# Performance work log

Measured on AMD Instinct MI355X. Metric: run time of the kernel, lower is better.

Reference implementation:

```python
import jax, jax.numpy as jnp
import numpy as np

TW = 25          # time_window
H = 128          # hidden_features
NL = 6           # hidden_layer
N = 8192         # batch*n_nodes
E = 131072       # edges (avg degree 16)
EDGE_DIM = 51    # 50 (u diff) + 1 (pos_x diff)
LEM_IN = 4       # pos_x, u_ch0, u_ch1, ts
PDE_L = 16.0
PDE_TMAX = 4.0
PDE_DT = 0.04
NEG_SLOPE = 0.2  # PyG GATConv leaky_relu slope


def swish(x):
    return x * jax.nn.sigmoid(x)


def setup_inputs() -> dict:
    key = jax.random.key(0)
    ks = jax.random.split(key, 32)
    def p(k, shape, s=0.05):
        return jax.random.normal(k, shape, jnp.float32) * s
    inp = {}
    inp['u'] = jax.random.normal(ks[0], (N, 2 * TW), jnp.float32)
    inp['pos'] = jax.random.uniform(ks[1], (N, 2), jnp.float32)
    inp['edge_index'] = jax.random.randint(ks[2], (2, E), 0, N)
    # LEM cell params (inp2hid: 4H, hid2hid: 3H, transform_z: H)
    inp['lem_inp_w'] = p(ks[3], (4 * H, LEM_IN)); inp['lem_inp_b'] = jnp.zeros(4 * H, jnp.float32)
    inp['lem_hid_w'] = p(ks[4], (3 * H, H));      inp['lem_hid_b'] = jnp.zeros(3 * H, jnp.float32)
    inp['lem_z_w'] = p(ks[5], (H, H));            inp['lem_z_b'] = jnp.zeros(H, jnp.float32)
    # lemoutput_mlp
    inp['mlp1_w'] = p(ks[6], (H, H)); inp['mlp1_b'] = jnp.zeros(H, jnp.float32)
    inp['mlp2_w'] = p(ks[7], (H, H)); inp['mlp2_b'] = jnp.zeros(H, jnp.float32)
    # main GAT layers (stacked over NL)
    inp['gnn_lin_w'] = p(ks[8], (NL, H, H)); inp['gnn_edge_w'] = p(ks[9], (NL, H, EDGE_DIM))
    inp['gnn_att_src'] = p(ks[10], (NL, H)); inp['gnn_att_dst'] = p(ks[11], (NL, H))
    inp['gnn_att_edge'] = p(ks[12], (NL, H)); inp['gnn_bias'] = jnp.zeros((NL, H), jnp.float32)
    # gate GAT layers
    inp['gate_lin_w'] = p(ks[13], (NL, H, H)); inp['gate_edge_w'] = p(ks[14], (NL, H, EDGE_DIM))
    inp['gate_att_src'] = p(ks[15], (NL, H)); inp['gate_att_dst'] = p(ks[16], (NL, H))
    inp['gate_att_edge'] = p(ks[17], (NL, H)); inp['gate_bias'] = jnp.zeros((NL, H), jnp.float32)
    # double_mlp + conv1d decoder (time_window==25 branch)
    inp['dbl_w'] = p(ks[18], (2 * H, H)); inp['dbl_b'] = jnp.zeros(2 * H, jnp.float32)
    inp['conv1_w'] = p(ks[19], (8, 2, 16)); inp['conv1_b'] = jnp.zeros(8, jnp.float32)
    inp['conv2_w'] = p(ks[20], (2, 8, 14)); inp['conv2_b'] = jnp.zeros(2, jnp.float32)
    return inp


def _gat(x, src, dst, edge_attr, lin_w, edge_w, a_src, a_dst, a_edge, bias):
    """Single-head GATConv with edge features (PyG semantics, aggregate at dst)."""
    xt = x @ lin_w.T                      # [N,H]
    et = edge_attr @ edge_w.T             # [E,H]
    logits = jax.nn.leaky_relu((xt @ a_src)[src] + (xt @ a_dst)[dst] + et @ a_edge, NEG_SLOPE)
    amax = jax.ops.segment_max(logits, dst, num_segments=N)
    amax = jnp.where(jnp.isfinite(amax), amax, 0.0)
    ex = jnp.exp(logits - amax[dst])
    denom = jax.ops.segment_sum(ex, dst, num_segments=N)
    w = ex / (denom[dst] + 1e-16)         # edge softmax over incoming edges
    out = jax.ops.segment_sum(w[:, None] * xt[src], dst, num_segments=N)
    return out + bias


def _forward(u, pos, lem_inp_w, lem_inp_b, lem_hid_w, lem_hid_b, lem_z_w, lem_z_b,
             mlp1_w, mlp1_b, mlp2_w, mlp2_b,
             gnn_lin_w, gnn_edge_w, gnn_att_src, gnn_att_dst, gnn_att_edge, gnn_bias,
             gate_lin_w, gate_edge_w, gate_att_src, gate_att_dst, gate_att_edge, gate_bias,
             dbl_w, dbl_b, conv1_w, conv1_b, conv2_w, conv2_b, edge_index):
    pos_x = pos[:, 1:2] / PDE_L    # [N,1]
    pos_t = pos[:, 0:1] / PDE_TMAX # [N,1]
    dt = jnp.cumsum(jnp.full((TW,), PDE_DT, jnp.float32))  # [TW]
    ts = pos_t + dt[None, :]       # [N,TW]
    # LEM input: [TW, N, 4] = (pos_x, u channel 0, u channel 1, ts)
    lem_x = jnp.concatenate([
        jnp.broadcast_to(pos_x[None, :, :], (TW, N, 1)),
        u[:, :TW].T[:, :, None],
        u[:, TW:].T[:, :, None],
        ts.T[:, :, None],
    ], axis=-1)

    def cell(carry, xt):
        y, z = carry
        ii = xt @ lem_inp_w.T + lem_inp_b   # [N,4H]
        hh = y @ lem_hid_w.T + lem_hid_b    # [N,3H]
        i1, i2, i3, i4 = jnp.split(ii, 4, axis=-1)
        h1, h2, h3 = jnp.split(hh, 3, axis=-1)
        ms_dt_bar = jax.nn.sigmoid(i1 + h1)
        ms_dt = jax.nn.sigmoid(i2 + h2)
        z = (1.0 - ms_dt) * z + ms_dt * jnp.tanh(i3 + h3)
        y = (1.0 - ms_dt_bar) * y + ms_dt_bar * jnp.tanh(z @ lem_z_w.T + lem_z_b + i4)
        return (y, z), None

    y0 = jnp.zeros((N, H), u.dtype)
    (y, _), _ = jax.lax.scan(cell, (y0, y0), lem_x)
    h = swish(y @ mlp1_w.T + mlp1_b)
    h = swish(h @ mlp2_w.T + mlp2_b)

    src, dst = edge_index[0], edge_index[1]
    edge_attr = jnp.concatenate([u[src] - u[dst], pos_x[src] - pos_x[dst]], axis=-1)  # [E,51]

    for i in range(NL):
        tau = jax.nn.sigmoid(_gat(h, src, dst, edge_attr, gate_lin_w[i], gate_edge_w[i],
                                  gate_att_src[i], gate_att_dst[i], gate_att_edge[i], gate_bias[i]))
        msg = swish(_gat(h, src, dst, edge_attr, gnn_lin_w[i], gnn_edge_w[i],
                         gnn_att_src[i], gnn_att_dst[i], gnn_att_edge[i], gnn_bias[i]))
        h = (1.0 - tau) * h + tau * msg

    h2 = swish(h @ dbl_w.T + dbl_b).reshape(N, 2, H)  # [N,2,128]
    dn = ('NCH', 'OIH', 'NCH')
    d = jax.lax.conv_general_dilated(h2, conv1_w, (3,), 'VALID', dimension_numbers=dn)
    d = swish(d + conv1_b[None, :, None])              # [N,8,38]
    d = jax.lax.conv_general_dilated(d, conv2_w, (1,), 'VALID', dimension_numbers=dn)
    d = d + conv2_b[None, :, None]                     # [N,2,25]
    out = u.reshape(N, 2, TW) + dt[None, None, :] * d
    return out.reshape(N, 2 * TW)


def reference(u, pos, edge_index, lem_inp_w, lem_inp_b, lem_hid_w, lem_hid_b, lem_z_w, lem_z_b,
              mlp1_w, mlp1_b, mlp2_w, mlp2_b,
              gnn_lin_w, gnn_edge_w, gnn_att_src, gnn_att_dst, gnn_att_edge, gnn_bias,
              gate_lin_w, gate_edge_w, gate_att_src, gate_att_dst, gate_att_edge, gate_bias,
              dbl_w, dbl_b, conv1_w, conv1_b, conv2_w, conv2_b):
    return _forward(u, pos, lem_inp_w, lem_inp_b, lem_hid_w, lem_hid_b, lem_z_w, lem_z_b,
                    mlp1_w, mlp1_b, mlp2_w, mlp2_b,
                    gnn_lin_w, gnn_edge_w, gnn_att_src, gnn_att_dst, gnn_att_edge, gnn_bias,
                    gate_lin_w, gate_edge_w, gate_att_src, gate_att_dst, gate_att_edge, gate_bias,
                    dbl_w, dbl_b, conv1_w, conv1_b, conv2_w, conv2_b, edge_index)
```

## Files before the change

kernel.cpp:

```cpp
#include <hip/hip_runtime.h>

#define N_NODES 8192
#define N_EDGES 131072

using short8 = __attribute__((ext_vector_type(8))) short;
using f32x4  = __attribute__((ext_vector_type(4))) float;

__device__ __forceinline__ float rcpf(float x){ return __builtin_amdgcn_rcpf(x); }
__device__ __forceinline__ float sigm(float x){ return rcpf(1.0f+__expf(-x)); }
__device__ __forceinline__ float ftanh(float x){ float e=__expf(2.0f*x); return (e-1.0f)*rcpf(e+1.0f); }
__device__ __forceinline__ float swishf(float x){ return x*sigm(x); }
__device__ __forceinline__ float leaky(float x){ return x>=0.0f? x : 0.2f*x; }
__device__ __forceinline__ float dot4(float4 a, float4 b){ return a.x*b.x+a.y*b.y+a.z*b.z+a.w*b.w; }
__device__ __forceinline__ short f2bf(float x){
  unsigned u=__float_as_uint(x);
  unsigned r=(u + 0x7fffu + ((u>>16)&1u))>>16;
  return (short)r;
}
__device__ __forceinline__ int cvtpk(float a, float b){
  int r; asm("v_cvt_pk_bf16_f32 %0, %1, %2" : "=v"(r) : "v"(a), "v"(b)); return r;
}

__device__ __forceinline__ float wave_rsum(float v){
  #pragma unroll
  for(int m=32;m;m>>=1) v+=__shfl_xor(v,m);
  return v;
}

__global__ __launch_bounds__(256) void hist_kernel(const int* __restrict__ dst, int* __restrict__ cnt){
  int e=blockIdx.x*256+threadIdx.x;
  if(e<N_EDGES) atomicAdd(&cnt[dst[e]],1);
}

__global__ __launch_bounds__(1024) void scan_kernel(const int* __restrict__ cnt, int* __restrict__ rowptr, int* __restrict__ cursor){
  __shared__ int sums[1024];
  int t=threadIdx.x; int base=t*8;
  int local[8]; int s=0;
  #pragma unroll
  for(int i=0;i<8;++i){ local[i]=s; s+=cnt[base+i]; }
  sums[t]=s; __syncthreads();
  for(int off=1;off<1024;off<<=1){
    int v=(t>=off)?sums[t-off]:0;
    __syncthreads();
    sums[t]+=v;
    __syncthreads();
  }
  int offset=(t>0)?sums[t-1]:0;
  #pragma unroll
  for(int i=0;i<8;++i){ int v=offset+local[i]; rowptr[base+i]=v; cursor[base+i]=v; }
  if(t==1023) rowptr[N_NODES]=sums[1023];
}

__global__ __launch_bounds__(256) void scatter_kernel(const int* __restrict__ src, const int* __restrict__ dst,
                                                      int* __restrict__ cursor, int* __restrict__ csr_src){
  int e=blockIdx.x*256+threadIdx.x;
  if(e<N_EDGES){
    int slot=atomicAdd(&cursor[dst[e]],1);
    csr_src[slot]=src[e];
  }
}

__global__ __launch_bounds__(256) void prep_bf16_kernel(
    const float* __restrict__ lem_hid_w, const float* __restrict__ lem_z_w,
    const float* __restrict__ mlp1_w, const float* __restrict__ mlp2_w,
    const float* __restrict__ gate_lin_w, const float* __restrict__ gnn_lin_w,
    const float* __restrict__ gate_ew, const float* __restrict__ gnn_ew,
    const float* __restrict__ gate_ae, const float* __restrict__ gnn_ae,
    short* __restrict__ whb, short* __restrict__ wzb, short* __restrict__ w1b,
    short* __restrict__ w2b, short* __restrict__ wlin16, float* __restrict__ we)
{
  int i=blockIdx.x*256+threadIdx.x;
  if(i<49152){ whb[i]=f2bf(lem_hid_w[i]); return; }
  if(i<65536){ int k=i-49152; wzb[k]=f2bf(lem_z_w[k]); return; }
  if(i<81920){ int k=i-65536; w1b[k]=f2bf(mlp1_w[k]); return; }
  if(i<98304){ int k=i-81920; w2b[k]=f2bf(mlp2_w[k]); return; }
  if(i<294912){
    int k=i-98304;
    int l=k>>15, which=(k>>14)&1, r=k&16383;
    const float* s = which? gnn_lin_w + l*16384 + r : gate_lin_w + l*16384 + r;
    wlin16[k]=f2bf(*s);
    return;
  }
  int idx=i-294912;
  if(idx>=12*51) return;
  int g=idx/51, k=idx%51, l=g>>1;
  const float* ew = (g&1)? gnn_ew + l*128*51 : gate_ew + l*128*51;
  const float* ae = (g&1)? gnn_ae + l*128    : gate_ae + l*128;
  float s=0.f;
  for(int f=0;f<128;++f) s+=ew[f*51+k]*ae[f];
  we[idx]=s;
}

__global__ __launch_bounds__(128) void gsc_kernel(const float* __restrict__ u, const float* __restrict__ pos,
                                                  const float* __restrict__ we, float* __restrict__ gsc){
  int n=blockIdx.x*128+threadIdx.x;
  float uv[50];
  #pragma unroll
  for(int k=0;k<50;++k) uv[k]=u[n*50+k];
  float px=pos[n*2+1]*(1.0f/16.0f);
  for(int g=0;g<12;++g){
    const float* w=we+g*51;
    float s=w[50]*px;
    #pragma unroll
    for(int k=0;k<50;++k) s+=w[k]*uv[k];
    gsc[g*N_NODES+n]=s;
  }
}

__device__ __forceinline__ void transform_phase(
    int tid, int n0,
    const short* __restrict__ h16, short* __restrict__ xts,
    float* __restrict__ ssred, float* __restrict__ sdred,
    const short* __restrict__ wl,
    const float* __restrict__ a_sg, const float* __restrict__ a_dg,
    const float* __restrict__ a_sm, const float* __restrict__ a_dm,
    const float* __restrict__ gsc_g, const float* __restrict__ gsc_m,
    short* __restrict__ xt_out, float* __restrict__ ss_out, float* __restrict__ sd_out)
{
  const int lane=tid&63, w=tid>>6;
  const int cg=w&1, ch=w>>1;
  const int r16=lane&15, kq=lane>>4;
  __syncthreads();
  short8 afr[4];
  #pragma unroll
  for(int kk=0;kk<4;++kk)
    afr[kk]=*(const short8*)&h16[r16*128 + ((kk*32+kq*8) ^ ((r16&7)<<3))];
  const short* wb = wl + cg*16384;
  const float* as_ = cg? a_sm : a_sg;
  const float* ad_ = cg? a_dm : a_dg;
  float ssp[4]={0,0,0,0}, sdp[4]={0,0,0,0};
  #pragma unroll
  for(int ci=0;ci<2;++ci){
    int c0=(ch*2+ci)*16;
    f32x4 acc={0.f,0.f,0.f,0.f};
    #pragma unroll
    for(int kk=0;kk<4;++kk){
      short8 b=*(const short8*)(wb + (c0+r16)*128 + kk*32 + kq*8);
      acc=__builtin_amdgcn_mfma_f32_16x16x32_bf16(afr[kk],b,acc,0,0,0);
    }
    float av=as_[c0+r16], dv=ad_[c0+r16];
    #pragma unroll
    for(int r=0;r<4;++r){
      ssp[r]+=acc[r]*av; sdp[r]+=acc[r]*dv;
      xts[(kq*4+r)*256 + cg*128 + c0 + r16]=f2bf(acc[r]);
    }
  }
  #pragma unroll
  for(int m=1;m<16;m<<=1){
    #pragma unroll
    for(int r=0;r<4;++r){ ssp[r]+=__shfl_xor(ssp[r],m); sdp[r]+=__shfl_xor(sdp[r],m); }
  }
  if(r16==0){
    #pragma unroll
    for(int r=0;r<4;++r){ ssred[w*16+kq*4+r]=ssp[r]; sdred[w*16+kq*4+r]=sdp[r]; }
  }
  __syncthreads();
  if(tid<32){
    int node=tid&15, cg2=tid>>4;
    float sv=0.f, dv=0.f;
    #pragma unroll
    for(int c2=0;c2<4;++c2){ sv+=ssred[(c2*2+cg2)*16+node]; dv+=sdred[(c2*2+cg2)*16+node]; }
    float gv=(cg2? gsc_m:gsc_g)[n0+node];
    ss_out[2*(n0+node)+cg2]=sv+gv;
    sd_out[2*(n0+node)+cg2]=dv-gv;
  }
  {
    const short8* sp=(const short8*)xts;
    short8* dp=(short8*)(xt_out + (size_t)n0*256);
    dp[tid]=sp[tid];
  }
}

__device__ __forceinline__ float4 aggregate_node(
    int n, int lane, float4* __restrict__ stgw,
    const int* __restrict__ rowptr, const int* __restrict__ csr_src,
    const short* __restrict__ xt_in, const float* __restrict__ ss_in, const float* __restrict__ sd_in,
    const float* __restrict__ bias_g, const float* __restrict__ bias_m,
    const float* __restrict__ h)
{
  const int s0=rowptr[n], deg=rowptr[n+1]-s0;
  const float2 sdv=*(const float2*)(sd_in+2*n);
  const float bg=sdv.x, bm=sdv.y;
  float4 hv={0.f,0.f,0.f,0.f};
  if(lane<32) hv=*(const float4*)(h + (size_t)n*128 + 4*lane);
  float dg=0.f,dm=0.f, acc0=0.f,acc1=0.f,acc2=0.f,acc3=0.f;
  for(int c=0;c<deg;c+=64){
    int i=c+lane, s=0; float eg=0.f, em=0.f;
    if(i<deg){
      s=csr_src[s0+i];
      float2 ssv=*(const float2*)(ss_in+2*s);
      eg=__expf(fminf(leaky(ssv.x+bg),60.f));
      em=__expf(fminf(leaky(ssv.y+bm),60.f));
      dg+=eg; dm+=em;
    }
    float4 st; st.x=__int_as_float(s); st.y=eg; st.z=em; st.w=0.f;
    stgw[lane]=st;
    __threadfence_block();
    int cnt=min(64,deg-c);
    for(int cb=0;cb<cnt;cb+=16){
      int sj[16]; float wj[16];
      #pragma unroll
      for(int j=0;j<16;++j){
        int idx=cb+j;
        float4 ev=stgw[idx<cnt? idx : cb];
        sj[j]=__float_as_int(ev.x);
        wj[j]=(idx<cnt)? (lane<32? ev.y : ev.z) : 0.f;
      }
      uint2 rows[16];
      #pragma unroll
      for(int j=0;j<16;++j)
        rows[j]=*(const uint2*)(xt_in + (size_t)sj[j]*256 + 4*lane);
      #pragma unroll
      for(int j=0;j<16;++j){
        float wv=wj[j];
        unsigned p0=rows[j].x, p1=rows[j].y;
        acc0+=wv*__uint_as_float(p0<<16);
        acc1+=wv*__uint_as_float(p0&0xffff0000u);
        acc2+=wv*__uint_as_float(p1<<16);
        acc3+=wv*__uint_as_float(p1&0xffff0000u);
      }
    }
  }
  dg=wave_rsum(dg); dm=wave_rsum(dm);
  float rr = lane<32? rcpf(dg+1e-16f) : rcpf(dm+1e-16f);
  const float* bp = lane<32? bias_g+4*lane : bias_m+4*(lane-32);
  float4 bv=*(const float4*)bp;
  float o0=acc0*rr+bv.x, o1=acc1*rr+bv.y, o2=acc2*rr+bv.z, o3=acc3*rr+bv.w;
  float s0_=sigm(o0), s1_=sigm(o1), s2_=sigm(o2), s3_=sigm(o3);
  float v0=lane<32? s0_:o0*s0_;
  float v1=lane<32? s1_:o1*s1_;
  float v2=lane<32? s2_:o2*s2_;
  float v3=lane<32? s3_:o3*s3_;
  float m0=__shfl_xor(v0,32), m1=__shfl_xor(v1,32), m2=__shfl_xor(v2,32), m3=__shfl_xor(v3,32);
  float4 r;
  if(lane<32){
    r.x=(1.0f-v0)*hv.x+v0*m0;
    r.y=(1.0f-v1)*hv.y+v1*m1;
    r.z=(1.0f-v2)*hv.z+v2*m2;
    r.w=(1.0f-v3)*hv.w+v3*m3;
  } else { r.x=r.y=r.z=r.w=0.f; }
  return r;
}

__global__ __launch_bounds__(512,2) void lem_t0_kernel(
    const float* __restrict__ u, const float* __restrict__ pos,
    const float* __restrict__ Wi, const float* __restrict__ bi,
    const short* __restrict__ whb, const float* __restrict__ bh,
    const short* __restrict__ wzb, const float* __restrict__ bz,
    const short* __restrict__ w1b, const float* __restrict__ b1,
    const short* __restrict__ w2b, const float* __restrict__ b2,
    float* __restrict__ hout,
    const short* __restrict__ wl,
    const float* __restrict__ a_sg, const float* __restrict__ a_dg,
    const float* __restrict__ a_sm, const float* __restrict__ a_dm,
    const float* __restrict__ gsc_g, const float* __restrict__ gsc_m,
    short* __restrict__ xt_out, float* __restrict__ ss_out, float* __restrict__ sd_out)
{
  __shared__ short y16[2][16*128];
  __shared__ short z16[2][16*128];
  __shared__ float u_s[32*50];
  __shared__ short h16[16*128];
  __shared__ short xts[16*256];
  __shared__ float ssred[128], sdred[128];

  const int tid=threadIdx.x, lane=tid&63, w=tid>>6;
  const int node=lane&15, q=lane>>4;
  const int n7=node&7;
  const int n0=blockIdx.x*32;

  for(int i=tid;i<32*50;i+=512) u_s[i]=u[n0*50+i];
  for(int i=tid;i<2*16*64;i+=512) ((int*)y16)[i]=0;

  const float px0=pos[(n0+node)*2+1]*(1.0f/16.0f),    pt0=pos[(n0+node)*2+0]*0.25f;
  const float px1=pos[(n0+16+node)*2+1]*(1.0f/16.0f), pt1=pos[(n0+16+node)*2+0]*0.25f;

  float bb[4][4], wix[4][4], wiw[4][4], wiy[4][4], wiz[4][4];
  #pragma unroll
  for(int gg=0; gg<4; ++gg){
    #pragma unroll
    for(int r=0;r<4;++r){
      int fr = w*16+q*4+r;
      int row = gg*128+fr;
      float4 wi = *(const float4*)(Wi+4*row);
      bb[gg][r] = bi[row] + ((gg<3)? bh[row] : bz[fr]);
      wix[gg][r]=wi.x; wiw[gg][r]=wi.w; wiy[gg][r]=wi.y; wiz[gg][r]=wi.z;
    }
  }

  short8 whf[3][4];
  #pragma unroll
  for(int gg=0;gg<3;++gg)
    #pragma unroll
    for(int kk=0;kk<4;++kk)
      whf[gg][kk]=*(const short8*)(whb + (gg*128 + w*16 + node)*128 + kk*32 + q*8);
  short8 wzf[4];
  #pragma unroll
  for(int kk=0;kk<4;++kk)
    wzf[kk]=*(const short8*)(wzb + (w*16 + node)*128 + kk*32 + q*8);

  float yr0[4]={0.f,0.f,0.f,0.f}, zr0[4]={0.f,0.f,0.f,0.f};
  float yr1[4]={0.f,0.f,0.f,0.f}, zr1[4]={0.f,0.f,0.f,0.f};
  float msb0[4], i4s0[4], msb1[4], i4s1[4];
  const int wrslot = (w*16+q*4) ^ (n7<<3);
  const int rdbase = n7<<3;
  __syncthreads();

  for(int t=0;t<25;++t){
    const float tf=(float)(t+1);
    {
      f32x4 h1a={0.f,0.f,0.f,0.f}, h2a=h1a, h3a=h1a;
      #pragma unroll
      for(int kk=0;kk<4;++kk){
        short8 yb=*(const short8*)&y16[0][node*128 + ((kk*32 + q*8) ^ rdbase)];
        h1a=__builtin_amdgcn_mfma_f32_16x16x32_bf16(whf[0][kk],yb,h1a,0,0,0);
        h2a=__builtin_amdgcn_mfma_f32_16x16x32_bf16(whf[1][kk],yb,h2a,0,0,0);
        h3a=__builtin_amdgcn_mfma_f32_16x16x32_bf16(whf[2][kk],yb,h3a,0,0,0);
      }
      const float u0=u_s[node*50+t], u1=u_s[node*50+25+t];
      const float ts=pt0+0.04f*tf;
      #pragma unroll
      for(int r=0;r<4;++r){
        float i1=bb[0][r]+wix[0][r]*px0+wiw[0][r]*ts+wiy[0][r]*u0+wiz[0][r]*u1;
        float i2=bb[1][r]+wix[1][r]*px0+wiw[1][r]*ts+wiy[1][r]*u0+wiz[1][r]*u1;
        float i3=bb[2][r]+wix[2][r]*px0+wiw[2][r]*ts+wiy[2][r]*u0+wiz[2][r]*u1;
        i4s0[r] =bb[3][r]+wix[3][r]*px0+wiw[3][r]*ts+wiy[3][r]*u0+wiz[3][r]*u1;
        msb0[r]=sigm(i1+h1a[r]);
        float ms=sigm(i2+h2a[r]);
        zr0[r]=(1.0f-ms)*zr0[r]+ms*ftanh(i3+h3a[r]);
      }
      int2 zz; zz.x=cvtpk(zr0[0],zr0[1]); zz.y=cvtpk(zr0[2],zr0[3]);
      *(int2*)&z16[0][node*128 + wrslot]=zz;
    }
    {
      f32x4 h1a={0.f,0.f,0.f,0.f}, h2a=h1a, h3a=h1a;
      #pragma unroll
      for(int kk=0;kk<4;++kk){
        short8 yb=*(const short8*)&y16[1][node*128 + ((kk*32 + q*8) ^ rdbase)];
        h1a=__builtin_amdgcn_mfma_f32_16x16x32_bf16(whf[0][kk],yb,h1a,0,0,0);
        h2a=__builtin_amdgcn_mfma_f32_16x16x32_bf16(whf[1][kk],yb,h2a,0,0,0);
        h3a=__builtin_amdgcn_mfma_f32_16x16x32_bf16(whf[2][kk],yb,h3a,0,0,0);
      }
      const float u0=u_s[(16+node)*50+t], u1=u_s[(16+node)*50+25+t];
      const float ts=pt1+0.04f*tf;
      #pragma unroll
      for(int r=0;r<4;++r){
        float i1=bb[0][r]+wix[0][r]*px1+wiw[0][r]*ts+wiy[0][r]*u0+wiz[0][r]*u1;
        float i2=bb[1][r]+wix[1][r]*px1+wiw[1][r]*ts+wiy[1][r]*u0+wiz[1][r]*u1;
        float i3=bb[2][r]+wix[2][r]*px1+wiw[2][r]*ts+wiy[2][r]*u0+wiz[2][r]*u1;
        i4s1[r] =bb[3][r]+wix[3][r]*px1+wiw[3][r]*ts+wiy[3][r]*u0+wiz[3][r]*u1;
        msb1[r]=sigm(i1+h1a[r]);
        float ms=sigm(i2+h2a[r]);
        zr1[r]=(1.0f-ms)*zr1[r]+ms*ftanh(i3+h3a[r]);
      }
      int2 zz; zz.x=cvtpk(zr1[0],zr1[1]); zz.y=cvtpk(zr1[2],zr1[3]);
      *(int2*)&z16[1][node*128 + wrslot]=zz;
    }
    __syncthreads();
    {
      f32x4 zw={0.f,0.f,0.f,0.f};
      #pragma unroll
      for(int kk=0;kk<4;++kk){
        short8 zb=*(const short8*)&z16[0][node*128 + ((kk*32 + q*8) ^ rdbase)];
        zw=__builtin_amdgcn_mfma_f32_16x16x32_bf16(wzf[kk],zb,zw,0,0,0);
      }
      #pragma unroll
      for(int r=0;r<4;++r)
        yr0[r]=(1.0f-msb0[r])*yr0[r]+msb0[r]*ftanh(zw[r]+i4s0[r]);
      int2 yy; yy.x=cvtpk(yr0[0],yr0[1]); yy.y=cvtpk(yr0[2],yr0[3]);
      *(int2*)&y16[0][node*128 + wrslot]=yy;
    }
    {
      f32x4 zw={0.f,0.f,0.f,0.f};
      #pragma unroll
      for(int kk=0;kk<4;++kk){
        short8 zb=*(const short8*)&z16[1][node*128 + ((kk*32 + q*8) ^ rdbase)];
        zw=__builtin_amdgcn_mfma_f32_16x16x32_bf16(wzf[kk],zb,zw,0,0,0);
      }
      #pragma unroll
      for(int r=0;r<4;++r)
        yr1[r]=(1.0f-msb1[r])*yr1[r]+msb1[r]*ftanh(zw[r]+i4s1[r]);
      int2 yy; yy.x=cvtpk(yr1[0],yr1[1]); yy.y=cvtpk(yr1[2],yr1[3]);
      *(int2*)&y16[1][node*128 + wrslot]=yy;
    }
    __syncthreads();
  }

  #pragma unroll
  for(int nt=0;nt<2;++nt){
    {
      short8 w1f[4];
      #pragma unroll
      for(int kk=0;kk<4;++kk)
        w1f[kk]=*(const short8*)(w1b + (w*16 + node)*128 + kk*32 + q*8);
      float4 b1v=*(const float4*)(b1 + w*16 + q*4);
      f32x4 a={0.f,0.f,0.f,0.f};
      #pragma unroll
      for(int kk=0;kk<4;++kk){
        short8 yb=*(const short8*)&y16[nt][node*128 + ((kk*32 + q*8) ^ rdbase)];
        a=__builtin_amdgcn_mfma_f32_16x16x32_bf16(w1f[kk],yb,a,0,0,0);
      }
      float t0=swishf(a[0]+b1v.x), t1=swishf(a[1]+b1v.y);
      float t2=swishf(a[2]+b1v.z), t3=swishf(a[3]+b1v.w);
      int2 zz; zz.x=cvtpk(t0,t1); zz.y=cvtpk(t2,t3);
      *(int2*)&z16[nt][node*128 + wrslot]=zz;
    }
    __syncthreads();
    {
      short8 w2f[4];
      #pragma unroll
      for(int kk=0;kk<4;++kk)
        w2f[kk]=*(const short8*)(w2b + (w*16 + node)*128 + kk*32 + q*8);
      float4 b2v=*(const float4*)(b2 + w*16 + q*4);
      f32x4 a={0.f,0.f,0.f,0.f};
      #pragma unroll
      for(int kk=0;kk<4;++kk){
        short8 zb=*(const short8*)&z16[nt][node*128 + ((kk*32 + q*8) ^ rdbase)];
        a=__builtin_amdgcn_mfma_f32_16x16x32_bf16(w2f[kk],zb,a,0,0,0);
      }
      float h0=swishf(a[0]+b2v.x), h1=swishf(a[1]+b2v.y);
      float h2=swishf(a[2]+b2v.z), h3=swishf(a[3]+b2v.w);
      float4 hv; hv.x=h0; hv.y=h1; hv.z=h2; hv.w=h3;
      *(float4*)(hout + (size_t)(n0+nt*16+node)*128 + w*16+q*4)=hv;
      int2 hb; hb.x=cvtpk(h0,h1); hb.y=cvtpk(h2,h3);
      *(int2*)&h16[node*128 + wrslot]=hb;
    }
    transform_phase(tid,n0+nt*16,h16,xts,ssred,sdred,wl,a_sg,a_dg,a_sm,a_dm,gsc_g,gsc_m,xt_out,ss_out,sd_out);
  }
}

__global__ __launch_bounds__(512,2) void gat_fused_kernel(
    const int* __restrict__ rowptr, const int* __restrict__ csr_src,
    const short* __restrict__ xt_in, const float* __restrict__ ss_in, const float* __restrict__ sd_in,
    const float* __restrict__ bias_g, const float* __restrict__ bias_m,
    float* __restrict__ h,
    const short* __restrict__ wl,
    const float* __restrict__ a_sg, const float* __restrict__ a_dg,
    const float* __restrict__ a_sm, const float* __restrict__ a_dm,
    const float* __restrict__ gsc_g, const float* __restrict__ gsc_m,
    short* __restrict__ xt_out, float* __restrict__ ss_out, float* __restrict__ sd_out)
{
  __shared__ short h16[16*128];
  __shared__ short xts[16*256];
  __shared__ float ssred[128], sdred[128];
  __shared__ float4 stg[8][64];
  const int tid=threadIdx.x, lane=tid&63, w=tid>>6;
  const int n0=blockIdx.x*16;
  #pragma unroll
  for(int which=0;which<2;++which){
    int row=w*2+which, n=n0+row;
    float4 hv=aggregate_node(n,lane,stg[w],rowptr,csr_src,xt_in,ss_in,sd_in,bias_g,bias_m,h);
    if(lane<32){
      *(float4*)(h+(size_t)n*128+4*lane)=hv;
      int2 hb; hb.x=cvtpk(hv.x,hv.y); hb.y=cvtpk(hv.z,hv.w);
      *(int2*)&h16[row*128 + ((4*lane) ^ ((row&7)<<3))]=hb;
    }
  }
  transform_phase(tid,n0,h16,xts,ssred,sdred,wl,a_sg,a_dg,a_sm,a_dm,gsc_g,gsc_m,xt_out,ss_out,sd_out);
}

__global__ __launch_bounds__(512,2) void gat_last_decoder_kernel(
    const int* __restrict__ rowptr, const int* __restrict__ csr_src,
    const short* __restrict__ xt_in, const float* __restrict__ ss_in, const float* __restrict__ sd_in,
    const float* __restrict__ bias_g, const float* __restrict__ bias_m,
    const float* __restrict__ h, const float* __restrict__ u,
    const float* __restrict__ Wd, const float* __restrict__ bd,
    const float* __restrict__ w1, const float* __restrict__ b1,
    const float* __restrict__ w2, const float* __restrict__ b2,
    float* __restrict__ out)
{
  __shared__ float hdec[16*128];
  __shared__ float h2[16][2][128];
  __shared__ float c1[16][8][38];
  __shared__ float w1s[256], w2s[224], b1s[8], b2s[2];
  __shared__ float4 stg[8][64];
  const int tid=threadIdx.x, lane=tid&63, w=tid>>6;
  const int n0=blockIdx.x*16;
  if(tid<256) w1s[tid]=w1[tid];
  else if(tid<480) w2s[tid-256]=w2[tid-256];
  else if(tid<488) b1s[tid-480]=b1[tid-480];
  else if(tid<490) b2s[tid-488]=b2[tid-488];
  #pragma unroll
  for(int which=0;which<2;++which){
    int row=w*2+which, n=n0+row;
    float4 hv=aggregate_node(n,lane,stg[w],rowptr,csr_src,xt_in,ss_in,sd_in,bias_g,bias_m,h);
    if(lane<32) *(float4*)&hdec[row*128+4*lane]=hv;
  }
  __syncthreads();
  {
    int o=tid&255, grp=tid>>8;
    const float4* wp=(const float4*)(Wd + o*128);
    float acc[8];
    #pragma unroll
    for(int n=0;n<8;++n) acc[n]=0.f;
    for(int k=0;k<32;++k){
      float4 wv=wp[k];
      #pragma unroll
      for(int n=0;n<8;++n){ float4 hval=*(const float4*)&hdec[(grp*8+n)*128+k*4]; acc[n]+=dot4(wv,hval); }
    }
    float bdv=bd[o];
    int chn=o>>7, p=o&127;
    #pragma unroll
    for(int n=0;n<8;++n) h2[grp*8+n][chn][p]=swishf(acc[n]+bdv);
  }
  __syncthreads();
  for(int idx=tid; idx<16*8*38; idx+=512){
    int n=idx/(8*38); int r=idx%(8*38); int oc=r/38, p=r%38;
    float acc=b1s[oc];
    const float* ww=&w1s[oc*32];
    #pragma unroll
    for(int ic=0;ic<2;++ic)
      #pragma unroll
      for(int k=0;k<16;++k) acc+=ww[ic*16+k]*h2[n][ic][3*p+k];
    c1[n][oc][p]=swishf(acc);
  }
  __syncthreads();
  for(int idx=tid; idx<16*2*25; idx+=512){
    int n=idx/50; int r=idx%50; int oc=r/25, p=r%25;
    float acc=b2s[oc];
    const float* ww=&w2s[oc*112];
    #pragma unroll
    for(int ic=0;ic<8;++ic)
      #pragma unroll
      for(int k=0;k<14;++k) acc+=ww[ic*14+k]*c1[n][ic][p+k];
    int col=oc*25+p;
    out[(n0+n)*50+col]=u[(n0+n)*50+col]+0.04f*(float)(p+1)*acc;
  }
}

extern "C" void kernel_launch(void* const* d_in, const int* in_sizes, int n_in,
                              void* d_out, int out_size, void* d_ws, size_t ws_size,
                              hipStream_t stream)
{
  const float* u          =(const float*)d_in[0];
  const float* pos        =(const float*)d_in[1];
  const int*   ei         =(const int*)d_in[2];
  const float* lem_inp_w  =(const float*)d_in[3];
  const float* lem_inp_b  =(const float*)d_in[4];
  const float* lem_hid_w  =(const float*)d_in[5];
  const float* lem_hid_b  =(const float*)d_in[6];
  const float* lem_z_w    =(const float*)d_in[7];
  const float* lem_z_b    =(const float*)d_in[8];
  const float* mlp1_w     =(const float*)d_in[9];
  const float* mlp1_b     =(const float*)d_in[10];
  const float* mlp2_w     =(const float*)d_in[11];
  const float* mlp2_b     =(const float*)d_in[12];
  const float* gnn_lin_w  =(const float*)d_in[13];
  const float* gnn_edge_w =(const float*)d_in[14];
  const float* gnn_att_src=(const float*)d_in[15];
  const float* gnn_att_dst=(const float*)d_in[16];
  const float* gnn_att_edge=(const float*)d_in[17];
  const float* gnn_bias   =(const float*)d_in[18];
  const float* gate_lin_w =(const float*)d_in[19];
  const float* gate_edge_w=(const float*)d_in[20];
  const float* gate_att_src=(const float*)d_in[21];
  const float* gate_att_dst=(const float*)d_in[22];
  const float* gate_att_edge=(const float*)d_in[23];
  const float* gate_bias  =(const float*)d_in[24];
  const float* dbl_w      =(const float*)d_in[25];
  const float* dbl_b      =(const float*)d_in[26];
  const float* conv1_w    =(const float*)d_in[27];
  const float* conv1_b    =(const float*)d_in[28];
  const float* conv2_w    =(const float*)d_in[29];
  const float* conv2_b    =(const float*)d_in[30];
  float* out=(float*)d_out;

  char* ws=(char*)d_ws;
  size_t off=0;
  auto alloc=[&](size_t bytes)->char*{ char* p=ws+off; off+=(bytes+255)&~(size_t)255; return p; };
  float* h    =(float*)alloc((size_t)N_NODES*128*4);
  short* xtA  =(short*)alloc((size_t)N_NODES*256*2);
  short* xtB  =(short*)alloc((size_t)N_NODES*256*2);
  float* ssA  =(float*)alloc((size_t)N_NODES*2*4);
  float* ssB  =(float*)alloc((size_t)N_NODES*2*4);
  float* sdA  =(float*)alloc((size_t)N_NODES*2*4);
  float* sdB  =(float*)alloc((size_t)N_NODES*2*4);
  float* gsc  =(float*)alloc((size_t)12*N_NODES*4);
  float* wearr=(float*)alloc(12*51*4);
  int* cnt    =(int*)alloc(N_NODES*4);
  int* rowptr =(int*)alloc((N_NODES+8)*4);
  int* cursor =(int*)alloc(N_NODES*4);
  int* csrsrc =(int*)alloc((size_t)N_EDGES*4);
  short* whb  =(short*)alloc(384*128*2);
  short* wzb  =(short*)alloc(128*128*2);
  short* w1b  =(short*)alloc(128*128*2);
  short* w2b  =(short*)alloc(128*128*2);
  short* wlin16=(short*)alloc((size_t)6*2*128*128*2);

  const int* src=ei;
  const int* dst=ei+N_EDGES;

  hipMemsetAsync(cnt,0,N_NODES*4,stream);
  hist_kernel<<<N_EDGES/256,256,0,stream>>>(dst,cnt);
  scan_kernel<<<1,1024,0,stream>>>(cnt,rowptr,cursor);
  scatter_kernel<<<N_EDGES/256,256,0,stream>>>(src,dst,cursor,csrsrc);
  prep_bf16_kernel<<<(294912+612+255)/256,256,0,stream>>>(lem_hid_w,lem_z_w,mlp1_w,mlp2_w,
                                                      gate_lin_w,gnn_lin_w,
                                                      gate_edge_w,gnn_edge_w,gate_att_edge,gnn_att_edge,
                                                      whb,wzb,w1b,w2b,wlin16,wearr);
  gsc_kernel<<<N_NODES/128,128,0,stream>>>(u,pos,wearr,gsc);

  short* xtbuf[2]={xtA,xtB};
  float* ssbuf[2]={ssA,ssB};
  float* sdbuf[2]={sdA,sdB};

  lem_t0_kernel<<<N_NODES/32,512,0,stream>>>(u,pos,lem_inp_w,lem_inp_b,whb,lem_hid_b,
      wzb,lem_z_b,w1b,mlp1_b,w2b,mlp2_b,h,
      wlin16,
      gate_att_src, gate_att_dst, gnn_att_src, gnn_att_dst,
      gsc, gsc+(size_t)N_NODES,
      xtbuf[0], ssbuf[0], sdbuf[0]);

  for(int l=0;l<5;++l){
    int in=l&1, o2=(l+1)&1;
    gat_fused_kernel<<<N_NODES/16,512,0,stream>>>(rowptr,csrsrc,
      xtbuf[in],ssbuf[in],sdbuf[in],
      gate_bias+l*128, gnn_bias+l*128, h,
      wlin16+(size_t)(l+1)*2*16384,
      gate_att_src+(l+1)*128, gate_att_dst+(l+1)*128,
      gnn_att_src+(l+1)*128, gnn_att_dst+(l+1)*128,
      gsc+(size_t)(2*(l+1))*N_NODES, gsc+(size_t)(2*(l+1)+1)*N_NODES,
      xtbuf[o2], ssbuf[o2], sdbuf[o2]);
  }

  gat_last_decoder_kernel<<<N_NODES/16,512,0,stream>>>(rowptr,csrsrc,
      xtbuf[1],ssbuf[1],sdbuf[1],
      gate_bias+5*128, gnn_bias+5*128, h, u,
      dbl_w, dbl_b, conv1_w, conv1_b, conv2_w, conv2_b, out);
}
```

Before: 362.8 us.

## Fuse all GAT layers and decoder into one cooperative persistent kernel

Replaces the five per-layer GAT launches and the decoder launch with a single cooperative kernel of 256 blocks. Each block keeps its 32 nodes' hidden state in shared memory and uses grid.sync between layers, which removes launch gaps and the global round-trips of h. The edge gather batch also shrinks from 16 to 8 rows to cut register pressure. The kernel depends on all 256 blocks being co-resident, and grid-wide barriers plus a larger shared-memory footprint can reduce occupancy. If the cooperative launch fails, the old multi-kernel path runs instead.

Result: no change. 356.8 us (-1.7%).

```diff
diff --git a/kernel.cpp b/kernel.cpp
--- a/kernel.cpp
+++ b/kernel.cpp
@@ -1,7 +1,10 @@
 #include <hip/hip_runtime.h>
+#include <hip/hip_cooperative_groups.h>
 
 #define N_NODES 8192
 #define N_EDGES 131072
+
+namespace cg = cooperative_groups;
 
 using short8 = __attribute__((ext_vector_type(8))) short;
 using f32x4  = __attribute__((ext_vector_type(4))) float;
@@ -118,16 +121,16 @@
     short* __restrict__ xt_out, float* __restrict__ ss_out, float* __restrict__ sd_out)
 {
   const int lane=tid&63, w=tid>>6;
-  const int cg=w&1, ch=w>>1;
+  const int cg_=w&1, ch=w>>1;
   const int r16=lane&15, kq=lane>>4;
   __syncthreads();
   short8 afr[4];
   #pragma unroll
   for(int kk=0;kk<4;++kk)
     afr[kk]=*(const short8*)&h16[r16*128 + ((kk*32+kq*8) ^ ((r16&7)<<3))];
-  const short* wb = wl + cg*16384;
-  const float* as_ = cg? a_sm : a_sg;
-  const float* ad_ = cg? a_dm : a_dg;
+  const short* wb = wl + cg_*16384;
+  const float* as_ = cg_? a_sm : a_sg;
+  const float* ad_ = cg_? a_dm : a_dg;
   float ssp[4]={0,0,0,0}, sdp[4]={0,0,0,0};
   #pragma unroll
   for(int ci=0;ci<2;++ci){
@@ -142,7 +145,7 @@
     #pragma unroll
     for(int r=0;r<4;++r){
       ssp[r]+=acc[r]*av; sdp[r]+=acc[r]*dv;
-      xts[(kq*4+r)*256 + cg*128 + c0 + r16]=f2bf(acc[r]);
+      xts[(kq*4+r)*256 + cg_*128 + c0 + r16]=f2bf(acc[r]);
     }
   }
   #pragma unroll
@@ -176,13 +179,11 @@
     const int* __restrict__ rowptr, const int* __restrict__ csr_src,
     const short* __restrict__ xt_in, const float* __restrict__ ss_in, const float* __restrict__ sd_in,
     const float* __restrict__ bias_g, const float* __restrict__ bias_m,
-    const float* __restrict__ h)
+    const float* __restrict__ hrow)
 {
   const int s0=rowptr[n], deg=rowptr[n+1]-s0;
   const float2 sdv=*(const float2*)(sd_in+2*n);
   const float bg=sdv.x, bm=sdv.y;
-  float4 hv={0.f,0.f,0.f,0.f};
-  if(lane<32) hv=*(const float4*)(h + (size_t)n*128 + 4*lane);
   float dg=0.f,dm=0.f, acc0=0.f,acc1=0.f,acc2=0.f,acc3=0.f;
   for(int c=0;c<deg;c+=64){
     int i=c+lane, s=0; float eg=0.f, em=0.f;
@@ -197,21 +198,21 @@
     stgw[lane]=st;
     __threadfence_block();
     int cnt=min(64,deg-c);
-    for(int cb=0;cb<cnt;cb+=16){
-      int sj[16]; float wj[16];
-      #pragma unroll
-      for(int j=0;j<16;++j){
+    for(int cb=0;cb<cnt;cb+=8){
+      int sj[8]; float wj[8];
+      #pragma unroll
+      for(int j=0;j<8;++j){
         int idx=cb+j;
         float4 ev=stgw[idx<cnt? idx : cb];
         sj[j]=__float_as_int(ev.x);
         wj[j]=(idx<cnt)? (lane<32? ev.y : ev.z) : 0.f;
       }
-      uint2 rows[16];
-      #pragma unroll
-      for(int j=0;j<16;++j)
+      uint2 rows[8];
+      #pragma unroll
+      for(int j=0;j<8;++j)
         rows[j]=*(const uint2*)(xt_in + (size_t)sj[j]*256 + 4*lane);
       #pragma unroll
-      for(int j=0;j<16;++j){
+      for(int j=0;j<8;++j){
         float wv=wj[j];
         unsigned p0=rows[j].x, p1=rows[j].y;
         acc0+=wv*__uint_as_float(p0<<16);
@@ -234,6 +235,7 @@
   float m0=__shfl_xor(v0,32), m1=__shfl_xor(v1,32), m2=__shfl_xor(v2,32), m3=__shfl_xor(v3,32);
   float4 r;
   if(lane<32){
+    float4 hv=*(const float4*)(hrow + 4*lane);
     r.x=(1.0f-v0)*hv.x+v0*m0;
     r.y=(1.0f-v1)*hv.y+v1*m1;
     r.z=(1.0f-v2)*hv.z+v2*m2;
@@ -428,6 +430,133 @@
   }
 }
 
+__global__ __launch_bounds__(512,2) void gnn_persist_kernel(
+    const int* __restrict__ rowptr, const int* __restrict__ csr_src,
+    const float* __restrict__ hin,
+    short* __restrict__ xtA, float* __restrict__ ssA, float* __restrict__ sdA,
+    short* __restrict__ xtB, float* __restrict__ ssB, float* __restrict__ sdB,
+    const short* __restrict__ wlin16,
+    const float* __restrict__ gate_att_src, const float* __restrict__ gate_att_dst,
+    const float* __restrict__ gnn_att_src, const float* __restrict__ gnn_att_dst,
+    const float* __restrict__ gsc,
+    const float* __restrict__ gate_bias, const float* __restrict__ gnn_bias,
+    const float* __restrict__ u,
+    const float* __restrict__ Wd, const float* __restrict__ bd,
+    const float* __restrict__ w1, const float* __restrict__ b1,
+    const float* __restrict__ w2, const float* __restrict__ b2,
+    float* __restrict__ out)
+{
+  __shared__ float hfp[32*128];
+  __shared__ union SM {
+    struct {
+      short h16[16*128];
+      short xts[16*256];
+      float ssred[128], sdred[128];
+      float4 stg[8][64];
+    } g;
+    struct {
+      float h2[16][2][128];
+      float c1[16][8][38];
+      float w1s[256], w2s[224], b1s[8], b2s[2];
+    } d;
+  } sm;
+
+  cg::grid_group grid = cg::this_grid();
+  const int tid=threadIdx.x, lane=tid&63, w=tid>>6;
+  const int n0=blockIdx.x*32;
+
+  for(int i=tid;i<32*128;i+=512) hfp[i]=hin[(size_t)n0*128+i];
+  __syncthreads();
+
+  for(int l=0;l<6;++l){
+    const short* xt_in = (l&1)? xtB : xtA;
+    const float* ss_in = (l&1)? ssB : ssA;
+    const float* sd_in = (l&1)? sdB : sdA;
+    const float* bias_g = gate_bias + l*128;
+    const float* bias_m = gnn_bias + l*128;
+    #pragma unroll
+    for(int nt=0;nt<2;++nt){
+      #pragma unroll
+      for(int which=0;which<2;++which){
+        int rl=w*2+which;
+        int row=nt*16+rl;
+        int n=n0+row;
+        float4 hv=aggregate_node(n,lane,sm.g.stg[w],rowptr,csr_src,xt_in,ss_in,sd_in,bias_g,bias_m,&hfp[row*128]);
+        if(lane<32){
+          *(float4*)&hfp[row*128+4*lane]=hv;
+          int2 hb; hb.x=cvtpk(hv.x,hv.y); hb.y=cvtpk(hv.z,hv.w);
+          *(int2*)&sm.g.h16[rl*128 + ((4*lane) ^ ((rl&7)<<3))]=hb;
+        }
+      }
+      if(l<5){
+        int lp=l+1;
+        transform_phase(tid,n0+nt*16,sm.g.h16,sm.g.xts,sm.g.ssred,sm.g.sdred,
+          wlin16+(size_t)lp*32768,
+          gate_att_src+lp*128, gate_att_dst+lp*128,
+          gnn_att_src+lp*128, gnn_att_dst+lp*128,
+          gsc+(size_t)(2*lp)*N_NODES, gsc+(size_t)(2*lp+1)*N_NODES,
+          (l&1)? xtA:xtB, (l&1)? ssA:ssB, (l&1)? sdA:sdB);
+      }
+    }
+    if(l<5){
+      __threadfence();
+      grid.sync();
+      __threadfence();
+    }
+  }
+
+  __syncthreads();
+  if(tid<256) sm.d.w1s[tid]=w1[tid];
+  else if(tid<480) sm.d.w2s[tid-256]=w2[tid-256];
+  else if(tid<488) sm.d.b1s[tid-480]=b1[tid-480];
+  else if(tid<490) sm.d.b2s[tid-488]=b2[tid-488];
+  __syncthreads();
+  for(int nt=0;nt<2;++nt){
+    const float* hbase=&hfp[nt*16*128];
+    {
+      int o=tid&255, grp=tid>>8;
+      const float4* wp=(const float4*)(Wd + o*128);
+      float acc[8];
+      #pragma unroll
+      for(int n=0;n<8;++n) acc[n]=0.f;
+      for(int k=0;k<32;++k){
+        float4 wv=wp[k];
+        #pragma unroll
+        for(int n=0;n<8;++n){ float4 hval=*(const float4*)&hbase[(grp*8+n)*128+k*4]; acc[n]+=dot4(wv,hval); }
+      }
+      float bdv=bd[o];
+      int chn=o>>7, p=o&127;
+      #pragma unroll
+      for(int n=0;n<8;++n) sm.d.h2[grp*8+n][chn][p]=swishf(acc[n]+bdv);
+    }
+    __syncthreads();
+    for(int idx=tid; idx<16*8*38; idx+=512){
+      int n=idx/(8*38); int r=idx%(8*38); int oc=r/38, p=r%38;
+      float acc=sm.d.b1s[oc];
+      const float* ww=&sm.d.w1s[oc*32];
+      #pragma unroll
+      for(int ic=0;ic<2;++ic)
+        #pragma unroll
+        for(int k=0;k<16;++k) acc+=ww[ic*16+k]*sm.d.h2[n][ic][3*p+k];
+      sm.d.c1[n][oc][p]=swishf(acc);
+    }
+    __syncthreads();
+    for(int idx=tid; idx<16*2*25; idx+=512){
+      int n=idx/50; int r=idx%50; int oc=r/25, p=r%25;
+      float acc=sm.d.b2s[oc];
+      const float* ww=&sm.d.w2s[oc*112];
+      #pragma unroll
+      for(int ic=0;ic<8;++ic)
+        #pragma unroll
+        for(int k=0;k<14;++k) acc+=ww[ic*14+k]*sm.d.c1[n][ic][p+k];
+      int col=oc*25+p;
+      int gn=n0+nt*16+n;
+      out[gn*50+col]=u[gn*50+col]+0.04f*(float)(p+1)*acc;
+    }
+    __syncthreads();
+  }
+}
+
 __global__ __launch_bounds__(512,2) void gat_fused_kernel(
     const int* __restrict__ rowptr, const int* __restrict__ csr_src,
     const short* __restrict__ xt_in, const float* __restrict__ ss_in, const float* __restrict__ sd_in,
@@ -448,7 +577,7 @@
   #pragma unroll
   for(int which=0;which<2;++which){
     int row=w*2+which, n=n0+row;
-    float4 hv=aggregate_node(n,lane,stg[w],rowptr,csr_src,xt_in,ss_in,sd_in,bias_g,bias_m,h);
+    float4 hv=aggregate_node(n,lane,stg[w],rowptr,csr_src,xt_in,ss_in,sd_in,bias_g,bias_m,h+(size_t)n*128);
     if(lane<32){
       *(float4*)(h+(size_t)n*128+4*lane)=hv;
       int2 hb; hb.x=cvtpk(hv.x,hv.y); hb.y=cvtpk(hv.z,hv.w);
@@ -482,7 +611,7 @@
   #pragma unroll
   for(int which=0;which<2;++which){
     int row=w*2+which, n=n0+row;
-    float4 hv=aggregate_node(n,lane,stg[w],rowptr,csr_src,xt_in,ss_in,sd_in,bias_g,bias_m,h);
+    float4 hv=aggregate_node(n,lane,stg[w],rowptr,csr_src,xt_in,ss_in,sd_in,bias_g,bias_m,h+(size_t)n*128);
     if(lane<32) *(float4*)&hdec[row*128+4*lane]=hv;
   }
   __syncthreads();
@@ -599,31 +728,58 @@
                                                       whb,wzb,w1b,w2b,wlin16,wearr);
   gsc_kernel<<<N_NODES/128,128,0,stream>>>(u,pos,wearr,gsc);
 
-  short* xtbuf[2]={xtA,xtB};
-  float* ssbuf[2]={ssA,ssB};
-  float* sdbuf[2]={sdA,sdB};
-
   lem_t0_kernel<<<N_NODES/32,512,0,stream>>>(u,pos,lem_inp_w,lem_inp_b,whb,lem_hid_b,
       wzb,lem_z_b,w1b,mlp1_b,w2b,mlp2_b,h,
       wlin16,
       gate_att_src, gate_att_dst, gnn_att_src, gnn_att_dst,
       gsc, gsc+(size_t)N_NODES,
-      xtbuf[0], ssbuf[0], sdbuf[0]);
+      xtA, ssA, sdA);
+
+  int occ=0;
+  hipError_t qerr=hipOccupancyMaxActiveBlocksPerMultiprocessor(&occ,
+      reinterpret_cast<const void*>(gnn_persist_kernel), 512, 0);
+  bool coop = (qerr==hipSuccess) && (occ>=1);
+
+  if(coop){
+    void* kargs[]={
+      (void*)&rowptr,(void*)&csrsrc,(void*)&h,
+      (void*)&xtA,(void*)&ssA,(void*)&sdA,
+      (void*)&xtB,(void*)&ssB,(void*)&sdB,
+      (void*)&wlin16,
+      (void*)&gate_att_src,(void*)&gate_att_dst,(void*)&gnn_att_src,(void*)&gnn_att_dst,
+      (void*)&gsc,
+      (void*)&gate_bias,(void*)&gnn_bias,
+      (void*)&u,(void*)&dbl_w,(void*)&dbl_b,
+      (void*)&conv1_w,(void*)&conv1_b,(void*)&conv2_w,(void*)&conv2_b,
+      (void*)&out
+    };
+    hipError_t lerr=hipLaunchCooperativeKernel((void*)gnn_persist_kernel,
+        dim3(N_NODES/32), dim3(512), kargs, 0, stream);
+    if(lerr==hipSuccess) return;
+  }
 
   for(int l=0;l<5;++l){
-    int in=l&1, o2=(l+1)&1;
-    gat_fused_kernel<<<N_NODES/16,512,0,stream>>>(rowptr,csrsrc,
-      xtbuf[in],ssbuf[in],sdbuf[in],
-      gate_bias+l*128, gnn_bias+l*128, h,
-      wlin16+(size_t)(l+1)*2*16384,
-      gate_att_src+(l+1)*128, gate_att_dst+(l+1)*128,
-      gnn_att_src+(l+1)*128, gnn_att_dst+(l+1)*128,
-      gsc+(size_t)(2*(l+1))*N_NODES, gsc+(size_t)(2*(l+1)+1)*N_NODES,
-      xtbuf[o2], ssbuf[o2], sdbuf[o2]);
-  }
-
-  gat_last_decoder_kernel<<<N_NODES/16,512,0,stream>>>(rowptr,csrsrc,
-      xtbuf[1],ssbuf[1],sdbuf[1],
-      gate_bias+5*128, gnn_bias+5*128, h, u,
-      dbl_w, dbl_b, conv1_w, conv1_b, conv2_w, conv2_b, out);
-}
+    short* xin = (l&1)? xtB:xtA;  float* sin_=(l&1)? ssA:ssA;
+    (void)xin; (void)sin_;
+  }
+  {
+    short* xtbuf[2]={xtA,xtB};
+    float* ssbuf[2]={ssA,ssB};
+    float* sdbuf[2]={sdA,sdB};
+    for(int l=0;l<5;++l){
+      int in=l&1, o2=(l+1)&1;
+      gat_fused_kernel<<<N_NODES/16,512,0,stream>>>(rowptr,csrsrc,
+        xtbuf[in],ssbuf[in],sdbuf[in],
+        gate_bias+l*128, gnn_bias+l*128, h,
+        wlin16+(size_t)(l+1)*2*16384,
+        gate_att_src+(l+1)*128, gate_att_dst+(l+1)*128,
+        gnn_att_src+(l+1)*128, gnn_att_dst+(l+1)*128,
+        gsc+(size_t)(2*(l+1))*N_NODES, gsc+(size_t)(2*(l+1)+1)*N_NODES,
+        xtbuf[o2], ssbuf[o2], sdbuf[o2]);
+    }
+    gat_last_decoder_kernel<<<N_NODES/16,512,0,stream>>>(rowptr,csrsrc,
+        xtbuf[1],ssbuf[1],sdbuf[1],
+        gate_bias+5*128, gnn_bias+5*128, h, u,
+        dbl_w, dbl_b, conv1_w, conv1_b, conv2_w, conv2_b, out);
+  }
+}
```
